# Optimization experiments

Hardware: AMD Instinct MI355X
Metric: run time of the kernel (lower is better)

The kernel has to match this reference:

```python
import jax, jax.numpy as jnp
import numpy as np

N_LAYERS = 3  # from init_kwargs


def setup_inputs() -> dict:
    key = jax.random.key(0)
    k1, k2, k3, k4, k5 = jax.random.split(key, 5)
    n_users, n_items, d = 200000, 100000, 64
    n_edges = 9600000
    N = n_users + n_items
    return {
        "user_emb": jax.random.normal(k1, (n_users, d), dtype=jnp.float32) * 0.1,
        "item_emb": jax.random.normal(k2, (n_items, d), dtype=jnp.float32) * 0.1,
        "edge_src": jax.random.randint(k3, (n_edges,), 0, N, dtype=jnp.int64),
        "edge_dst": jax.random.randint(k4, (n_edges,), 0, N, dtype=jnp.int64),
        "edge_val": jax.random.uniform(k5, (n_edges,), dtype=jnp.float32),
    }


def _spmm(edge_src, edge_dst, edge_val, x, num_nodes):
    # out[i] = sum_{e: dst[e]==i} val[e] * x[src[e]]  (sparse.mm with COO graph)
    msgs = edge_val[:, None] * x[edge_src]  # [E, D]
    return jax.ops.segment_sum(msgs, edge_dst, num_segments=num_nodes)


def reference(user_emb, item_emb, edge_src, edge_dst, edge_val):
    n_users = user_emb.shape[0]
    N = n_users + item_emb.shape[0]
    all_emb = jnp.concatenate([user_emb, item_emb], axis=0)  # [N, D]
    acc = all_emb  # running sum over layers (equivalent to stack + mean)
    h = all_emb
    for _ in range(N_LAYERS):
        h = _spmm(edge_src, edge_dst, edge_val, h, N)
        acc = acc + h
    light_out = acc / jnp.asarray(N_LAYERS + 1, dtype=acc.dtype)
    users = light_out[:n_users]
    items = light_out[n_users:]
    return users, items
```

## Files before the change

### kernel.cpp

```cpp
#include <hip/hip_runtime.h>


static constexpr int D     = 64;
static constexpr int BLK   = 256;
static constexpr int WPB   = BLK / 64;
static constexpr int CHUNK = 16384;
static constexpr int NBK   = 512;
static constexpr int MAXNB = 1024;

typedef unsigned long long u64;
typedef unsigned short u16;

__device__ __forceinline__ float4 ldf4(const float* p) {
    return *reinterpret_cast<const float4*>(p);
}
__device__ __forceinline__ u16 f2b(float f) {
    unsigned u = __float_as_uint(f);
    return (u16)((u + 0x7FFFu + ((u >> 16) & 1u)) >> 16);
}
__device__ __forceinline__ float b2f(u16 h) {
    return __uint_as_float((unsigned)h << 16);
}
__device__ __forceinline__ float blo(unsigned u) {
    return __uint_as_float(u << 16);
}
__device__ __forceinline__ float bhi(unsigned u) {
    return __uint_as_float(u & 0xFFFF0000u);
}

__global__ __launch_bounds__(512)
void p_hist(const int* __restrict__ edst, unsigned* __restrict__ cnt,
            int E, int NB, int nchunk) {
    __shared__ unsigned h[MAXNB];
    const int c = blockIdx.x;
    for (int j = threadIdx.x; j < NB; j += 512) h[j] = 0u;
    __syncthreads();
    const long long base = (long long)c * CHUNK;
    const int lim = (int)min((long long)CHUNK, (long long)E - base);
    const int nv = lim >> 2;
    const int4* d4 = (const int4*)(edst + base);
    for (int i = threadIdx.x; i < nv; i += 512) {
        int4 d = d4[i];
        atomicAdd(&h[(unsigned)d.x >> 9], 1u);
        atomicAdd(&h[(unsigned)d.y >> 9], 1u);
        atomicAdd(&h[(unsigned)d.z >> 9], 1u);
        atomicAdd(&h[(unsigned)d.w >> 9], 1u);
    }
    for (int i = (nv << 2) + threadIdx.x; i < lim; i += 512)
        atomicAdd(&h[(unsigned)edst[base + i] >> 9], 1u);
    __syncthreads();
    for (int j = threadIdx.x; j < NB; j += 512)
        cnt[(size_t)j * nchunk + c] = h[j];
}

__global__ __launch_bounds__(1024)
void p_reduce(const unsigned* __restrict__ cnt, unsigned* __restrict__ bsum, int M) {
    __shared__ unsigned wsum[16];
    int i = blockIdx.x * 1024 + threadIdx.x;
    unsigned v = (i < M) ? cnt[i] : 0u;
    #pragma unroll
    for (int d = 1; d < 64; d <<= 1) v += __shfl_xor(v, d);
    if ((threadIdx.x & 63) == 0) wsum[threadIdx.x >> 6] = v;
    __syncthreads();
    if (threadIdx.x < 16) {
        unsigned x = wsum[threadIdx.x];
        #pragma unroll
        for (int d = 1; d < 16; d <<= 1) x += __shfl_xor(x, d);
        if (threadIdx.x == 0) bsum[blockIdx.x] = x;
    }
}

__global__ __launch_bounds__(1024)
void k_scan(const unsigned* __restrict__ cnt, unsigned* __restrict__ off, int N) {
    __shared__ unsigned wsum[16];
    __shared__ unsigned carry_s;
    const int lane = threadIdx.x & 63;
    const int w    = threadIdx.x >> 6;
    if (threadIdx.x == 0) carry_s = 0;
    __syncthreads();
    for (int base = 0; base < N; base += 1024) {
        int i = base + (int)threadIdx.x;
        unsigned v = (i < N) ? cnt[i] : 0u;
        unsigned inc = v;
        #pragma unroll
        for (int d = 1; d < 64; d <<= 1) {
            unsigned t = __shfl_up(inc, d);
            if (lane >= d) inc += t;
        }
        if (lane == 63) wsum[w] = inc;
        __syncthreads();
        if (threadIdx.x < 16) {
            unsigned x = wsum[threadIdx.x];
            #pragma unroll
            for (int d = 1; d < 16; d <<= 1) {
                unsigned t = __shfl_up(x, d);
                if ((int)threadIdx.x >= d) x += t;
            }
            wsum[threadIdx.x] = x;
        }
        __syncthreads();
        unsigned carry = carry_s;
        unsigned woff  = (w == 0) ? 0u : wsum[w - 1];
        if (i < N) off[i] = carry + woff + inc - v;
        __syncthreads();
        if (threadIdx.x == 1023) carry_s = carry + wsum[15];
        __syncthreads();
    }
    if (threadIdx.x == 0) off[N] = carry_s;
}

__global__ __launch_bounds__(1024)
void p_scanapply(unsigned* __restrict__ cnt, const unsigned* __restrict__ bsumX, int M) {
    __shared__ unsigned wsum[16];
    const int lane = threadIdx.x & 63;
    const int w    = threadIdx.x >> 6;
    int i = blockIdx.x * 1024 + threadIdx.x;
    unsigned v = (i < M) ? cnt[i] : 0u;
    unsigned inc = v;
    #pragma unroll
    for (int d = 1; d < 64; d <<= 1) {
        unsigned t = __shfl_up(inc, d);
        if (lane >= d) inc += t;
    }
    if (lane == 63) wsum[w] = inc;
    __syncthreads();
    if (threadIdx.x < 16) {
        unsigned x = wsum[threadIdx.x];
        #pragma unroll
        for (int d = 1; d < 16; d <<= 1) {
            unsigned t = __shfl_up(x, d);
            if ((int)threadIdx.x >= d) x += t;
        }
        wsum[threadIdx.x] = x;
    }
    __syncthreads();
    unsigned excl = inc - v + ((w == 0) ? 0u : wsum[w - 1]) + bsumX[blockIdx.x];
    if (i < M) cnt[i] = excl;
}

__device__ __forceinline__ void part1(unsigned s, unsigned d, float v,
                                      unsigned* cur, u64* __restrict__ tmp) {
    unsigned b  = d >> 9;
    unsigned dl = d & (NBK - 1);
    unsigned pos = atomicAdd(&cur[b], 1u);
    tmp[pos] = ((u64)((dl << 19) | s) << 32) | __float_as_uint(v);
}

__global__ __launch_bounds__(512)
void p_part(const int* __restrict__ esrc, const int* __restrict__ edst,
            const float* __restrict__ ev, const unsigned* __restrict__ cnt,
            u64* __restrict__ tmp, int E, int NB, int nchunk) {
    __shared__ unsigned cur[MAXNB];
    const int c = blockIdx.x;
    for (int j = threadIdx.x; j < NB; j += 512)
        cur[j] = cnt[(size_t)j * nchunk + c];
    __syncthreads();
    const long long base = (long long)c * CHUNK;
    const int lim = (int)min((long long)CHUNK, (long long)E - base);
    const int nv = lim >> 2;
    const int4*   s4 = (const int4*)(esrc + base);
    const int4*   d4 = (const int4*)(edst + base);
    const float4* v4 = (const float4*)(ev + base);
    for (int i = threadIdx.x; i < nv; i += 512) {
        int4 ss = s4[i]; int4 dd = d4[i]; float4 vv = v4[i];
        part1((unsigned)ss.x, (unsigned)dd.x, vv.x, cur, tmp);
        part1((unsigned)ss.y, (unsigned)dd.y, vv.y, cur, tmp);
        part1((unsigned)ss.z, (unsigned)dd.z, vv.z, cur, tmp);
        part1((unsigned)ss.w, (unsigned)dd.w, vv.w, cur, tmp);
    }
    for (int i = (nv << 2) + threadIdx.x; i < lim; i += 512)
        part1((unsigned)esrc[base + i], (unsigned)edst[base + i], ev[base + i], cur, tmp);
}

__global__ __launch_bounds__(512)
void p_bsort(const u64* __restrict__ tmp, const unsigned* __restrict__ cnt,
             u64* __restrict__ fin, unsigned* __restrict__ off,
             int E, int N, int NB, int nchunk) {
    __shared__ unsigned c2[NBK];
    __shared__ unsigned o2[NBK];
    __shared__ unsigned ws8[8];
    const int b = blockIdx.x, tid = threadIdx.x;
    const int lane = tid & 63, w = tid >> 6;
    const unsigned base = cnt[(size_t)b * nchunk];
    const unsigned end  = (b + 1 < NB) ? cnt[(size_t)(b + 1) * nchunk] : (unsigned)E;
    c2[tid] = 0u;
    __syncthreads();
    for (unsigned i = base + tid; i < end; i += 512) {
        unsigned dl = (unsigned)(tmp[i] >> 51) & (NBK - 1);
        atomicAdd(&c2[dl], 1u);
    }
    __syncthreads();
    unsigned v = c2[tid], inc = v;
    #pragma unroll
    for (int d = 1; d < 64; d <<= 1) { unsigned t = __shfl_up(inc, d); if (lane >= d) inc += t; }
    if (lane == 63) ws8[w] = inc;
    __syncthreads();
    if (tid < 8) {
        unsigned x = ws8[tid];
        #pragma unroll
        for (int d = 1; d < 8; d <<= 1) { unsigned t = __shfl_up(x, d); if (tid >= d) x += t; }
        ws8[tid] = x;
    }
    __syncthreads();
    const unsigned excl = inc - v + ((w == 0) ? 0u : ws8[w - 1]);
    const unsigned mybase = base + excl;
    o2[tid] = mybase;
    int n0 = b * NBK + tid;
    if (n0 < N) off[n0] = mybase;
    if (b == 0 && tid == 0) off[N] = (unsigned)E;
    __syncthreads();
    for (unsigned i = base + tid; i < end; i += 512) {
        u64 pk = tmp[i];
        unsigned dl  = (unsigned)(pk >> 51) & (NBK - 1);
        unsigned src = (unsigned)(pk >> 32) & 0x7FFFFu;
        unsigned vb  = (unsigned)pk;
        unsigned pos = atomicAdd(&o2[dl], 1u);
        fin[pos] = (u64)src | ((u64)vb << 32);
    }
}

__global__ __launch_bounds__(BLK)
void k_cvt(const float* __restrict__ ue, const float* __restrict__ ie,
           u16* __restrict__ x0, long long u_elems, long long total4) {
    long long i = (long long)blockIdx.x * BLK + threadIdx.x;
    if (i >= total4) return;
    long long idx = i * 4;
    float4 b = (idx < u_elems) ? ldf4(ue + idx) : ldf4(ie + (idx - u_elems));
    ushort4 o;
    o.x = f2b(b.x); o.y = f2b(b.y); o.z = f2b(b.z); o.w = f2b(b.w);
    *reinterpret_cast<ushort4*>(x0 + idx) = o;
}

template<int FINAL>
__global__ __launch_bounds__(BLK)
void g_gather(const unsigned* __restrict__ off, const u64* __restrict__ edges,
              const u16* __restrict__ x, u16* __restrict__ hout,
              const float* __restrict__ ue, const float* __restrict__ ie,
              const u16* __restrict__ h1, const u16* __restrict__ h2,
              int n_users, float* __restrict__ out, int N) {
    __shared__ u64 sh[WPB][64];
    const int w    = threadIdx.x >> 6;
    const int lane = threadIdx.x & 63;
    const int node = blockIdx.x * WPB + w;
    if (node >= N) return;
    const int q  = lane >> 3;
    const int d8 = lane & 7;
    const unsigned beg = off[node];
    const unsigned end = off[node + 1];
    float a0=0.f,a1=0.f,a2=0.f,a3=0.f,a4=0.f,a5=0.f,a6=0.f,a7=0.f;
    for (unsigned base = beg; base < end; base += 64) {
        const int cnt = (int)min(64u, end - base);
        sh[w][lane] = (lane < cnt) ? __builtin_nontemporal_load(&edges[base + lane])
                                   : 0ull;
        const int npad = (cnt + 7) & ~7;
        int j = 0;
        for (; j + 32 <= npad; j += 32) {
            u64 p0 = sh[w][j      + q];
            u64 p1 = sh[w][j +  8 + q];
            u64 p2 = sh[w][j + 16 + q];
            u64 p3 = sh[w][j + 24 + q];
            const uint4 x0v = *reinterpret_cast<const uint4*>(x + (size_t)(unsigned)p0 * D + d8 * 8);
            const uint4 x1v = *reinterpret_cast<const uint4*>(x + (size_t)(unsigned)p1 * D + d8 * 8);
            const uint4 x2v = *reinterpret_cast<const uint4*>(x + (size_t)(unsigned)p2 * D + d8 * 8);
            const uint4 x3v = *reinterpret_cast<const uint4*>(x + (size_t)(unsigned)p3 * D + d8 * 8);
            float v0 = __uint_as_float((unsigned)(p0 >> 32));
            float v1 = __uint_as_float((unsigned)(p1 >> 32));
            float v2 = __uint_as_float((unsigned)(p2 >> 32));
            float v3 = __uint_as_float((unsigned)(p3 >> 32));
            a0 += v0*blo(x0v.x); a1 += v0*bhi(x0v.x); a2 += v0*blo(x0v.y); a3 += v0*bhi(x0v.y);
            a4 += v0*blo(x0v.z); a5 += v0*bhi(x0v.z); a6 += v0*blo(x0v.w); a7 += v0*bhi(x0v.w);
            a0 += v1*blo(x1v.x); a1 += v1*bhi(x1v.x); a2 += v1*blo(x1v.y); a3 += v1*bhi(x1v.y);
            a4 += v1*blo(x1v.z); a5 += v1*bhi(x1v.z); a6 += v1*blo(x1v.w); a7 += v1*bhi(x1v.w);
            a0 += v2*blo(x2v.x); a1 += v2*bhi(x2v.x); a2 += v2*blo(x2v.y); a3 += v2*bhi(x2v.y);
            a4 += v2*blo(x2v.z); a5 += v2*bhi(x2v.z); a6 += v2*blo(x2v.w); a7 += v2*bhi(x2v.w);
            a0 += v3*blo(x3v.x); a1 += v3*bhi(x3v.x); a2 += v3*blo(x3v.y); a3 += v3*bhi(x3v.y);
            a4 += v3*blo(x3v.z); a5 += v3*bhi(x3v.z); a6 += v3*blo(x3v.w); a7 += v3*bhi(x3v.w);
        }
        for (; j < npad; j += 8) {
            u64 p = sh[w][j + q];
            const uint4 xv = *reinterpret_cast<const uint4*>(x + (size_t)(unsigned)p * D + d8 * 8);
            float v = __uint_as_float((unsigned)(p >> 32));
            a0 += v*blo(xv.x); a1 += v*bhi(xv.x); a2 += v*blo(xv.y); a3 += v*bhi(xv.y);
            a4 += v*blo(xv.z); a5 += v*bhi(xv.z); a6 += v*blo(xv.w); a7 += v*bhi(xv.w);
        }
    }
    #pragma unroll
    for (int m = 8; m < 64; m <<= 1) {
        a0 += __shfl_xor(a0, m); a1 += __shfl_xor(a1, m);
        a2 += __shfl_xor(a2, m); a3 += __shfl_xor(a3, m);
        a4 += __shfl_xor(a4, m); a5 += __shfl_xor(a5, m);
        a6 += __shfl_xor(a6, m); a7 += __shfl_xor(a7, m);
    }
    if (lane < 8) {
        const size_t o = (size_t)node * D + (size_t)d8 * 8;
        if (FINAL) {
            const float* h0row = (node < n_users) ? (ue + (size_t)node * D)
                                                  : (ie + (size_t)(node - n_users) * D);
            float4 hA = ldf4(h0row + d8 * 8);
            float4 hB = ldf4(h0row + d8 * 8 + 4);
            uint4 r1 = *reinterpret_cast<const uint4*>(h1 + o);
            uint4 r2 = *reinterpret_cast<const uint4*>(h2 + o);
            float4 oA, oB;
            oA.x = (hA.x + blo(r1.x) + blo(r2.x) + a0) * 0.25f;
            oA.y = (hA.y + bhi(r1.x) + bhi(r2.x) + a1) * 0.25f;
            oA.z = (hA.z + blo(r1.y) + blo(r2.y) + a2) * 0.25f;
            oA.w = (hA.w + bhi(r1.y) + bhi(r2.y) + a3) * 0.25f;
            oB.x = (hB.x + blo(r1.z) + blo(r2.z) + a4) * 0.25f;
            oB.y = (hB.y + bhi(r1.z) + bhi(r2.z) + a5) * 0.25f;
            oB.z = (hB.z + blo(r1.w) + blo(r2.w) + a6) * 0.25f;
            oB.w = (hB.w + bhi(r1.w) + bhi(r2.w) + a7) * 0.25f;
            *reinterpret_cast<float4*>(out + o)     = oA;
            *reinterpret_cast<float4*>(out + o + 4) = oB;
        } else {
            uint4 hv;
            hv.x = ((unsigned)f2b(a1) << 16) | f2b(a0);
            hv.y = ((unsigned)f2b(a3) << 16) | f2b(a2);
            hv.z = ((unsigned)f2b(a5) << 16) | f2b(a4);
            hv.w = ((unsigned)f2b(a7) << 16) | f2b(a6);
            *reinterpret_cast<uint4*>(hout + o) = hv;
        }
    }
}

__global__ __launch_bounds__(BLK)
void scatter_first(const int* __restrict__ esrc, const int* __restrict__ edst,
                   const float* __restrict__ ev,
                   const float* __restrict__ ue, const float* __restrict__ ie,
                   int n_users, float* __restrict__ y, int n_edges) {
    long long t = (long long)blockIdx.x * BLK + threadIdx.x;
    int e = (int)(t >> 4);
    if (e >= n_edges) return;
    int lane = (int)(threadIdx.x & 15);
    int s = esrc[e]; int d = edst[e]; float v = ev[e];
    const float* xrow = (s < n_users) ? (ue + (size_t)s * D)
                                      : (ie + (size_t)(s - n_users) * D);
    float4 xs = ldf4(xrow + lane * 4);
    float* yp = y + (size_t)d * D + lane * 4;
    unsafeAtomicAdd(yp + 0, v * xs.x);
    unsafeAtomicAdd(yp + 1, v * xs.y);
    unsafeAtomicAdd(yp + 2, v * xs.z);
    unsafeAtomicAdd(yp + 3, v * xs.w);
}

__global__ __launch_bounds__(BLK)
void scatter_gen(const int* __restrict__ esrc, const int* __restrict__ edst,
                 const float* __restrict__ ev, const float* __restrict__ x,
                 float* __restrict__ y, int n_edges) {
    long long t = (long long)blockIdx.x * BLK + threadIdx.x;
    int e = (int)(t >> 4);
    if (e >= n_edges) return;
    int lane = (int)(threadIdx.x & 15);
    int s = esrc[e]; int d = edst[e]; float v = ev[e];
    float4 xs = ldf4(x + (size_t)s * D + lane * 4);
    float* yp = y + (size_t)d * D + lane * 4;
    unsafeAtomicAdd(yp + 0, v * xs.x);
    unsafeAtomicAdd(yp + 1, v * xs.y);
    unsafeAtomicAdd(yp + 2, v * xs.z);
    unsafeAtomicAdd(yp + 3, v * xs.w);
}

__global__ __launch_bounds__(BLK)
void combine4(const float* __restrict__ ue, const float* __restrict__ ie,
              const float* __restrict__ h1, const float* __restrict__ h2,
              const float* __restrict__ h3, float* __restrict__ out,
              long long u_elems, long long total4) {
    long long i = (long long)blockIdx.x * BLK + threadIdx.x;
    if (i >= total4) return;
    long long idx = i * 4;
    float4 b  = (idx < u_elems) ? ldf4(ue + idx) : ldf4(ie + (idx - u_elems));
    float4 a1 = ldf4(h1 + idx);
    float4 a2 = ldf4(h2 + idx);
    float4 a3 = ldf4(h3 + idx);
    float4 r;
    r.x = (b.x + a1.x + a2.x + a3.x) * 0.25f;
    r.y = (b.y + a1.y + a2.y + a3.y) * 0.25f;
    r.z = (b.z + a1.z + a2.z + a3.z) * 0.25f;
    r.w = (b.w + a1.w + a2.w + a3.w) * 0.25f;
    *reinterpret_cast<float4*>(out + idx) = r;
}

extern "C" void kernel_launch(void* const* d_in, const int* in_sizes, int n_in,
                              void* d_out, int out_size, void* d_ws, size_t ws_size,
                              hipStream_t stream) {
    const float* ue   = (const float*)d_in[0];
    const float* ie   = (const float*)d_in[1];
    const int*   esrc = (const int*)d_in[2];
    const int*   edst = (const int*)d_in[3];
    const float* ev   = (const float*)d_in[4];

    const int n_users = in_sizes[0] / D;
    const int n_items = in_sizes[1] / D;
    const int E       = in_sizes[2];
    const int N       = n_users + n_items;
    const long long elems = (long long)N * D;
    const size_t bufBytes = (size_t)elems * sizeof(float);

    const int NB     = (N + NBK - 1) / NBK;
    const int nchunk = (E + CHUNK - 1) / CHUNK;
    const int M      = NB * nchunk;
    const int nb1    = (M + 1023) / 1024;

    const long long total4  = elems / 4;
    const int vecBlocks     = (int)((total4 + BLK - 1) / BLK);
    const long long u_elems = (long long)n_users * D;
    const int gBlocks       = (N + WPB - 1) / WPB;
    float* out = (float*)d_out;

    const size_t tmpBytes = (size_t)E * 8;
    const size_t hbBytes  = (size_t)elems * 2;
    char* p = (char*)d_ws;
    u64* tmp = (u64*)p;  u16* x0 = (u16*)p;   p += (tmpBytes > hbBytes ? tmpBytes : hbBytes);
    u16*      h1b  = (u16*)p;                 p += hbBytes;
    u16*      h2b  = (u16*)p;                 p += hbBytes;
    u64*      fin  = (u64*)p;                 p += tmpBytes;
    unsigned* cnt  = (unsigned*)p;            p += (size_t)M * 4;
    unsigned* off  = (unsigned*)p;            p += ((size_t)N + 1) * 4;
    unsigned* bsum = (unsigned*)p;            p += (size_t)nb1 * 4;
    unsigned* bsumX= (unsigned*)p;            p += ((size_t)nb1 + 1) * 4;
    const size_t need = (size_t)(p - (char*)d_ws);

    if (ws_size >= need && NB <= MAXNB && N < (1 << 19)) {
        p_hist<<<nchunk, 512, 0, stream>>>(edst, cnt, E, NB, nchunk);
        p_reduce<<<nb1, 1024, 0, stream>>>(cnt, bsum, M);
        k_scan<<<1, 1024, 0, stream>>>(bsum, bsumX, nb1);
        p_scanapply<<<nb1, 1024, 0, stream>>>(cnt, bsumX, M);
        p_part<<<nchunk, 512, 0, stream>>>(esrc, edst, ev, cnt, tmp, E, NB, nchunk);
        p_bsort<<<NB, 512, 0, stream>>>(tmp, cnt, fin, off, E, N, NB, nchunk);
        k_cvt<<<vecBlocks, BLK, 0, stream>>>(ue, ie, x0, u_elems, total4);
        g_gather<0><<<gBlocks, BLK, 0, stream>>>(off, fin, x0, h1b, ue, ie,
                                                 nullptr, nullptr, n_users, nullptr, N);
        g_gather<0><<<gBlocks, BLK, 0, stream>>>(off, fin, h1b, h2b, ue, ie,
                                                 nullptr, nullptr, n_users, nullptr, N);
        g_gather<1><<<gBlocks, BLK, 0, stream>>>(off, fin, h2b, nullptr, ue, ie,
                                                 h1b, h2b, n_users, out, N);
    } else {
        float* h1 = (float*)d_ws;
        float* h2 = (float*)((char*)d_ws + bufBytes);
        float* h3 = (float*)((char*)d_ws + 2 * bufBytes);
        const int scatterBlocks = (int)(((long long)E * 16 + BLK - 1) / BLK);
        hipMemsetAsync(h1, 0, bufBytes, stream);
        hipMemsetAsync(h2, 0, bufBytes, stream);
        hipMemsetAsync(h3, 0, bufBytes, stream);
        scatter_first<<<scatterBlocks, BLK, 0, stream>>>(esrc, edst, ev, ue, ie,
                                                         n_users, h1, E);
        scatter_gen<<<scatterBlocks, BLK, 0, stream>>>(esrc, edst, ev, h1, h2, E);
        scatter_gen<<<scatterBlocks, BLK, 0, stream>>>(esrc, edst, ev, h2, h3, E);
        combine4<<<vecBlocks, BLK, 0, stream>>>(ue, ie, h1, h2, h3, out,
                                                u_elems, total4);
    }
}
```

Measured before the change: 952.0 us.

## Stage partition and bucket sort through shared-memory permutations; fuse bf16 convert into partition

The partition kernel now builds a per-chunk local histogram and permutation in LDS, so each block writes its edges to global memory in bucket order, in contiguous runs, instead of scattering them through atomics. The bucket sort does the same with an LDS permutation when the bucket fits, so its output writes are sequential. The separate fp32-to-bf16 conversion kernel is folded into extra blocks of the partition launch, and workspace buffers are aliased to shrink the footprint. The cost is more LDS per block (about 80KB in p_part), which lowers occupancy, plus re-reading the edge arrays within each chunk. Aliasing h2b onto x0 is only safe because x0 is dead after the first gather.

```diff
diff --git a/kernel.cpp b/kernel.cpp
--- a/kernel.cpp
+++ b/kernel.cpp
@@ -7,6 +7,8 @@
 static constexpr int CHUNK = 16384;
 static constexpr int NBK   = 512;
 static constexpr int MAXNB = 1024;
+static constexpr int PERMCAP = 18432;
+static constexpr int CVTB  = 256;
 
 typedef unsigned long long u64;
 typedef unsigned short u16;
@@ -17,9 +19,6 @@
 __device__ __forceinline__ u16 f2b(float f) {
     unsigned u = __float_as_uint(f);
     return (u16)((u + 0x7FFFu + ((u >> 16) & 1u)) >> 16);
-}
-__device__ __forceinline__ float b2f(u16 h) {
-    return __uint_as_float((unsigned)h << 16);
 }
 __device__ __forceinline__ float blo(unsigned u) {
     return __uint_as_float(u << 16);
@@ -138,38 +137,101 @@
     if (i < M) cnt[i] = excl;
 }
 
-__device__ __forceinline__ void part1(unsigned s, unsigned d, float v,
-                                      unsigned* cur, u64* __restrict__ tmp) {
-    unsigned b  = d >> 9;
-    unsigned dl = d & (NBK - 1);
-    unsigned pos = atomicAdd(&cur[b], 1u);
-    tmp[pos] = ((u64)((dl << 19) | s) << 32) | __float_as_uint(v);
-}
-
 __global__ __launch_bounds__(512)
 void p_part(const int* __restrict__ esrc, const int* __restrict__ edst,
             const float* __restrict__ ev, const unsigned* __restrict__ cnt,
-            u64* __restrict__ tmp, int E, int NB, int nchunk) {
-    __shared__ unsigned cur[MAXNB];
+            u64* __restrict__ tmp,
+            const float* __restrict__ ue, const float* __restrict__ ie,
+            u16* __restrict__ x0, long long u_elems, long long total4,
+            int E, int NB, int nchunk) {
+    if ((int)blockIdx.x >= nchunk) {
+        const long long stride = (long long)CVTB * 512;
+        for (long long i = (long long)(blockIdx.x - nchunk) * 512 + threadIdx.x;
+             i < total4; i += stride) {
+            long long idx = i * 4;
+            float4 b = (idx < u_elems) ? ldf4(ue + idx) : ldf4(ie + (idx - u_elems));
+            ushort4 o;
+            o.x = f2b(b.x); o.y = f2b(b.y); o.z = f2b(b.z); o.w = f2b(b.w);
+            *reinterpret_cast<ushort4*>(x0 + idx) = o;
+        }
+        return;
+    }
+    __shared__ unsigned lhist[MAXNB];
+    __shared__ unsigned lbase[MAXNB];
+    __shared__ unsigned lcur[MAXNB];
+    __shared__ unsigned gbase[MAXNB];
+    __shared__ unsigned perm[CHUNK];
+    __shared__ unsigned ws8s[8];
+    __shared__ unsigned carry_s;
     const int c = blockIdx.x;
-    for (int j = threadIdx.x; j < NB; j += 512)
-        cur[j] = cnt[(size_t)j * nchunk + c];
+    const int lane = threadIdx.x & 63, w = threadIdx.x >> 6;
+    for (int j = threadIdx.x; j < NB; j += 512) lhist[j] = 0u;
+    if (threadIdx.x == 0) carry_s = 0u;
     __syncthreads();
     const long long base = (long long)c * CHUNK;
     const int lim = (int)min((long long)CHUNK, (long long)E - base);
-    const int nv = lim >> 2;
-    const int4*   s4 = (const int4*)(esrc + base);
-    const int4*   d4 = (const int4*)(edst + base);
-    const float4* v4 = (const float4*)(ev + base);
-    for (int i = threadIdx.x; i < nv; i += 512) {
-        int4 ss = s4[i]; int4 dd = d4[i]; float4 vv = v4[i];
-        part1((unsigned)ss.x, (unsigned)dd.x, vv.x, cur, tmp);
-        part1((unsigned)ss.y, (unsigned)dd.y, vv.y, cur, tmp);
-        part1((unsigned)ss.z, (unsigned)dd.z, vv.z, cur, tmp);
-        part1((unsigned)ss.w, (unsigned)dd.w, vv.w, cur, tmp);
-    }
-    for (int i = (nv << 2) + threadIdx.x; i < lim; i += 512)
-        part1((unsigned)esrc[base + i], (unsigned)edst[base + i], ev[base + i], cur, tmp);
+    {
+        const int nv = lim >> 2;
+        const int4* d4 = (const int4*)(edst + base);
+        for (int i = threadIdx.x; i < nv; i += 512) {
+            int4 d = d4[i];
+            atomicAdd(&lhist[(unsigned)d.x >> 9], 1u);
+            atomicAdd(&lhist[(unsigned)d.y >> 9], 1u);
+            atomicAdd(&lhist[(unsigned)d.z >> 9], 1u);
+            atomicAdd(&lhist[(unsigned)d.w >> 9], 1u);
+        }
+        for (int i = (nv << 2) + threadIdx.x; i < lim; i += 512)
+            atomicAdd(&lhist[(unsigned)edst[base + i] >> 9], 1u);
+    }
+    __syncthreads();
+    for (int b0 = 0; b0 < NB; b0 += 512) {
+        int j = b0 + (int)threadIdx.x;
+        unsigned v = (j < NB) ? lhist[j] : 0u;
+        unsigned inc = v;
+        #pragma unroll
+        for (int d = 1; d < 64; d <<= 1) {
+            unsigned t = __shfl_up(inc, d);
+            if (lane >= d) inc += t;
+        }
+        if (lane == 63) ws8s[w] = inc;
+        __syncthreads();
+        if (threadIdx.x < 8) {
+            unsigned x = ws8s[threadIdx.x];
+            #pragma unroll
+            for (int d = 1; d < 8; d <<= 1) {
+                unsigned t = __shfl_up(x, d);
+                if ((int)threadIdx.x >= d) x += t;
+            }
+            ws8s[threadIdx.x] = x;
+        }
+        __syncthreads();
+        unsigned carry = carry_s;
+        if (j < NB) {
+            unsigned e = carry + ((w == 0) ? 0u : ws8s[w - 1]) + inc - v;
+            lbase[j] = e;
+            lcur[j]  = e;
+            gbase[j] = cnt[(size_t)j * nchunk + c];
+        }
+        __syncthreads();
+        if (threadIdx.x == 511) carry_s = carry + ws8s[7];
+        __syncthreads();
+    }
+    for (int i = threadIdx.x; i < lim; i += 512) {
+        unsigned d = (unsigned)edst[base + i];
+        unsigned r = atomicAdd(&lcur[d >> 9], 1u);
+        perm[r] = (unsigned)i;
+    }
+    __syncthreads();
+    for (int t = threadIdx.x; t < lim; t += 512) {
+        unsigned i  = perm[t];
+        unsigned d  = (unsigned)edst[base + i];
+        unsigned s  = (unsigned)esrc[base + i];
+        unsigned vb = __float_as_uint(ev[base + i]);
+        unsigned b  = d >> 9;
+        unsigned dl = d & (NBK - 1);
+        unsigned g  = gbase[b] + ((unsigned)t - lbase[b]);
+        tmp[g] = ((u64)((dl << 19) | s) << 32) | vb;
+    }
 }
 
 __global__ __launch_bounds__(512)
@@ -178,57 +240,59 @@
              int E, int N, int NB, int nchunk) {
     __shared__ unsigned c2[NBK];
     __shared__ unsigned o2[NBK];
-    __shared__ unsigned ws8[8];
+    __shared__ unsigned ws8s[8];
+    __shared__ unsigned perm[PERMCAP];
     const int b = blockIdx.x, tid = threadIdx.x;
     const int lane = tid & 63, w = tid >> 6;
     const unsigned base = cnt[(size_t)b * nchunk];
     const unsigned end  = (b + 1 < NB) ? cnt[(size_t)(b + 1) * nchunk] : (unsigned)E;
+    const unsigned m = end - base;
     c2[tid] = 0u;
     __syncthreads();
-    for (unsigned i = base + tid; i < end; i += 512) {
-        unsigned dl = (unsigned)(tmp[i] >> 51) & (NBK - 1);
-        atomicAdd(&c2[dl], 1u);
-    }
+    for (unsigned i = base + tid; i < end; i += 512)
+        atomicAdd(&c2[(unsigned)(tmp[i] >> 51) & (NBK - 1)], 1u);
     __syncthreads();
     unsigned v = c2[tid], inc = v;
     #pragma unroll
     for (int d = 1; d < 64; d <<= 1) { unsigned t = __shfl_up(inc, d); if (lane >= d) inc += t; }
-    if (lane == 63) ws8[w] = inc;
+    if (lane == 63) ws8s[w] = inc;
     __syncthreads();
     if (tid < 8) {
-        unsigned x = ws8[tid];
+        unsigned x = ws8s[tid];
         #pragma unroll
         for (int d = 1; d < 8; d <<= 1) { unsigned t = __shfl_up(x, d); if (tid >= d) x += t; }
-        ws8[tid] = x;
-    }
-    __syncthreads();
-    const unsigned excl = inc - v + ((w == 0) ? 0u : ws8[w - 1]);
-    const unsigned mybase = base + excl;
-    o2[tid] = mybase;
+        ws8s[tid] = x;
+    }
+    __syncthreads();
+    const unsigned excl = inc - v + ((w == 0) ? 0u : ws8s[w - 1]);
+    o2[tid] = excl;
     int n0 = b * NBK + tid;
-    if (n0 < N) off[n0] = mybase;
+    if (n0 < N) off[n0] = base + excl;
     if (b == 0 && tid == 0) off[N] = (unsigned)E;
     __syncthreads();
-    for (unsigned i = base + tid; i < end; i += 512) {
-        u64 pk = tmp[i];
-        unsigned dl  = (unsigned)(pk >> 51) & (NBK - 1);
-        unsigned src = (unsigned)(pk >> 32) & 0x7FFFFu;
-        unsigned vb  = (unsigned)pk;
-        unsigned pos = atomicAdd(&o2[dl], 1u);
-        fin[pos] = (u64)src | ((u64)vb << 32);
-    }
-}
-
-__global__ __launch_bounds__(BLK)
-void k_cvt(const float* __restrict__ ue, const float* __restrict__ ie,
-           u16* __restrict__ x0, long long u_elems, long long total4) {
-    long long i = (long long)blockIdx.x * BLK + threadIdx.x;
-    if (i >= total4) return;
-    long long idx = i * 4;
-    float4 b = (idx < u_elems) ? ldf4(ue + idx) : ldf4(ie + (idx - u_elems));
-    ushort4 o;
-    o.x = f2b(b.x); o.y = f2b(b.y); o.z = f2b(b.z); o.w = f2b(b.w);
-    *reinterpret_cast<ushort4*>(x0 + idx) = o;
+    if (m <= (unsigned)PERMCAP) {
+        for (unsigned i = base + tid; i < end; i += 512) {
+            unsigned dl = (unsigned)(tmp[i] >> 51) & (NBK - 1);
+            unsigned r  = atomicAdd(&o2[dl], 1u);
+            perm[r] = i - base;
+        }
+        __syncthreads();
+        for (unsigned t = tid; t < m; t += 512) {
+            u64 pk = tmp[base + perm[t]];
+            unsigned src = (unsigned)(pk >> 32) & 0x7FFFFu;
+            unsigned vb  = (unsigned)pk;
+            fin[base + t] = (u64)src | ((u64)vb << 32);
+        }
+    } else {
+        for (unsigned i = base + tid; i < end; i += 512) {
+            u64 pk = tmp[i];
+            unsigned dl  = (unsigned)(pk >> 51) & (NBK - 1);
+            unsigned src = (unsigned)(pk >> 32) & 0x7FFFFu;
+            unsigned vb  = (unsigned)pk;
+            unsigned r   = atomicAdd(&o2[dl], 1u);
+            fin[base + r] = (u64)src | ((u64)vb << 32);
+        }
+    }
 }
 
 template<int FINAL>
@@ -408,11 +472,11 @@
 
     const size_t tmpBytes = (size_t)E * 8;
     const size_t hbBytes  = (size_t)elems * 2;
+    const size_t r1Bytes  = tmpBytes > hbBytes ? tmpBytes : hbBytes;
     char* p = (char*)d_ws;
-    u64* tmp = (u64*)p;  u16* x0 = (u16*)p;   p += (tmpBytes > hbBytes ? tmpBytes : hbBytes);
-    u16*      h1b  = (u16*)p;                 p += hbBytes;
-    u16*      h2b  = (u16*)p;                 p += hbBytes;
+    u64* tmp = (u64*)p;  u16* h1b = (u16*)p;  p += r1Bytes;
     u64*      fin  = (u64*)p;                 p += tmpBytes;
+    u16*      x0   = (u16*)p; u16* h2b = x0;  p += hbBytes;
     unsigned* cnt  = (unsigned*)p;            p += (size_t)M * 4;
     unsigned* off  = (unsigned*)p;            p += ((size_t)N + 1) * 4;
     unsigned* bsum = (unsigned*)p;            p += (size_t)nb1 * 4;
@@ -424,9 +488,10 @@
         p_reduce<<<nb1, 1024, 0, stream>>>(cnt, bsum, M);
         k_scan<<<1, 1024, 0, stream>>>(bsum, bsumX, nb1);
         p_scanapply<<<nb1, 1024, 0, stream>>>(cnt, bsumX, M);
-        p_part<<<nchunk, 512, 0, stream>>>(esrc, edst, ev, cnt, tmp, E, NB, nchunk);
+        p_part<<<nchunk + CVTB, 512, 0, stream>>>(esrc, edst, ev, cnt, tmp,
+                                                  ue, ie, x0, u_elems, total4,
+                                                  E, NB, nchunk);
         p_bsort<<<NB, 512, 0, stream>>>(tmp, cnt, fin, off, E, N, NB, nchunk);
-        k_cvt<<<vecBlocks, BLK, 0, stream>>>(ue, ie, x0, u_elems, total4);
         g_gather<0><<<gBlocks, BLK, 0, stream>>>(off, fin, x0, h1b, ue, ie,
                                                  nullptr, nullptr, n_users, nullptr, N);
         g_gather<0><<<gBlocks, BLK, 0, stream>>>(off, fin, h1b, h2b, ue, ie,
```

After: 1.141 ms. +19.9%, slower.
